# Kernel optimization log

Hardware: AMD Instinct MI355X
Metric: run time of the kernel (lower is better)

The kernel has to match this reference:

```python
import jax, jax.numpy as jnp
import numpy as np

SX, SY, C, K = 256, 256, 3, 15
DD, DT, SIGMA = 5, 0.2, 0.65
C0 = tuple(i % C for i in range(K))
C1 = tuple(tuple(i for i in range(K) if i % C == c) for c in range(C))
MA = DD - SIGMA  # flow magnitude bound


def _sobel(A):
    # A: (X, Y, c) -> (X, Y, 2, c); matches jsp.signal.convolve2d(..., mode='same')
    kx = jnp.array([[1., 0., -1.], [2., 0., -2.], [1., 0., -1.]], dtype=A.dtype)
    ky = kx.T
    # convolve2d flips the kernel; emulate true convolution by correlating with rot180 kernels
    kern = jnp.stack([jnp.rot90(ky, 2), jnp.rot90(kx, 2)])[:, None]  # (2,1,3,3): [grad_y, grad_x]
    x = jnp.transpose(A, (2, 0, 1))[:, None]                          # (c,1,X,Y)
    out = jax.lax.conv_general_dilated(x, kern, (1, 1), 'SAME')       # (c,2,X,Y)
    return jnp.transpose(out, (2, 3, 1, 0))                           # (X,Y,2,c)


def _reintegration(A, P, F):
    # Reintegration tracking, has_hidden=True, border='wall', mix='softmax'
    xs, ys = jnp.meshgrid(jnp.arange(SX), jnp.arange(SY))
    pos = (jnp.dstack((ys, xs)) + .5).astype(A.dtype)     # (X,Y,2) cell centers (row, col)
    mus = pos[..., None] + jnp.clip(DT * F, -MA, MA)      # (X,Y,2,C) target centers
    mus = jnp.clip(mus, SIGMA, SX - SIGMA)                # wall border
    shifts = jnp.array([(dx, dy) for dx in range(-DD, DD + 1) for dy in range(-DD, DD + 1)])
    cap = min(1., 2 * SIGMA)

    def step(sft):
        sh = (sft[0], sft[1])
        Ar = jnp.roll(A, sh, axis=(0, 1))
        Pr = jnp.roll(P, sh, axis=(0, 1))
        mur = jnp.roll(mus, sh, axis=(0, 1))
        dpmu = jnp.abs(pos[..., None] - mur)              # (X,Y,2,C)
        sz = .5 - dpmu + SIGMA
        area = jnp.prod(jnp.clip(sz, 0., cap), axis=2) / (4 * SIGMA ** 2)  # (X,Y,C)
        return Ar * area, Pr

    nA, nP = jax.vmap(step)(shifts)                       # (N,X,Y,C), (N,X,Y,K)
    expnA = jnp.exp(nA.sum(-1, keepdims=True)) - 1.       # softmax mix rule
    newA = nA.sum(0)
    newP = (nP * expnA).sum(0) / (expnA.sum(0) + 1e-10)
    return newA, newP


def _forward(A, P, fK_real, fK_imag, m, s):
    fK = fK_real + 1j * fK_imag                           # (X,Y,K) kernel FFTs
    fA = jnp.fft.fft2(A, axes=(0, 1))                     # (X,Y,C)
    fAk = jnp.take(fA, jnp.array(C0), axis=2)             # (X,Y,K) per-kernel source channel
    U = jnp.real(jnp.fft.ifft2(fK * fAk, axes=(0, 1)))    # (X,Y,K)
    U = (2. * jnp.exp(-((U - m) ** 2) / (2. * s ** 2)) - 1.) * P  # growth(U,m,s)*P
    U = jnp.dstack([U[:, :, C1[c]].sum(-1) for c in range(C)])    # (X,Y,C)
    F = _sobel(U)                                         # (X,Y,2,C)
    Cg = _sobel(A.sum(-1, keepdims=True))                 # (X,Y,2,1)
    alpha = jnp.clip((A[:, :, None, :] / 2.) ** 2, 0., 1.)
    F = jnp.clip(F * (1. - alpha) - Cg * alpha, -MA, MA)
    return _reintegration(A, P, F)


def setup_inputs() -> dict:
    key = jax.random.key(0)
    kA, kP, kr, km, ks, ka, kb, kw = jax.random.split(key, 8)
    A = jax.random.uniform(kA, (SX, SY, C), dtype=jnp.float32)
    P = jax.random.uniform(kP, (SX, SY, K), dtype=jnp.float32)
    R = 15.0
    r = jax.random.uniform(kr, (K,), minval=.2, maxval=1.)
    m = jax.random.uniform(km, (K,), minval=.05, maxval=.5, dtype=jnp.float32)
    s = jax.random.uniform(ks, (K,), minval=.001, maxval=.18, dtype=jnp.float32)
    a = jax.random.uniform(ka, (K, 3))
    b = jax.random.uniform(kb, (K, 3), minval=.001, maxval=1.)
    w = jax.random.uniform(kw, (K, 3), minval=.01, maxval=.5)
    mid = SX // 2
    D = jnp.linalg.norm(jnp.mgrid[-mid:mid, -mid:mid], axis=0)[..., None] / ((R + 15.) * r)  # (X,Y,K)
    Kk = jax.nn.sigmoid(-(D - 1.) * 10.) * (b * jnp.exp(-((D[..., None] - a) / w) ** 2)).sum(-1)
    nK = Kk / Kk.sum((0, 1), keepdims=True)
    fK = jnp.fft.fft2(jnp.fft.fftshift(nK, axes=(0, 1)), axes=(0, 1))
    return {"A": A, "P": P,
            "fK_real": jnp.real(fK).astype(jnp.float32),
            "fK_imag": jnp.imag(fK).astype(jnp.float32),
            "m": m, "s": s}


def reference(A, P, fK_real, fK_imag, m, s):
    return _forward(A, P, fK_real, fK_imag, m, s)
```

## Files before the change

kernel.cpp:

```cpp
#include <hip/hip_runtime.h>


#define SXY 256
#define XY  65536
#define NC  3
#define NK  15

__device__ __forceinline__ float2 cmul(float2 a, float2 b) {
  return make_float2(a.x * b.x - a.y * b.y, a.x * b.y + a.y * b.x);
}

__device__ __forceinline__ void fft256_lds(float2* b0, float2* b1, int t, float sign) {
  float2* src = b0;
  float2* dst = b1;
#pragma unroll
  for (int stage = 0; stage < 4; ++stage) {
    __syncthreads();
    const int Ns = 1 << (2 * stage);
    float2 v0 = src[t];
    float2 v1 = src[t + 64];
    float2 v2 = src[t + 128];
    float2 v3 = src[t + 192];
    const int jm = t & (Ns - 1);
    float ang = sign * 6.283185307179586f * (float)jm / (float)(Ns * 4);
    float sn, cs;
    __sincosf(ang, &sn, &cs);
    float2 w1 = make_float2(cs, sn);
    float2 w2 = cmul(w1, w1);
    float2 w3 = cmul(w2, w1);
    v1 = cmul(v1, w1);
    v2 = cmul(v2, w2);
    v3 = cmul(v3, w3);
    float2 a0 = make_float2(v0.x + v2.x, v0.y + v2.y);
    float2 a1 = make_float2(v0.x - v2.x, v0.y - v2.y);
    float2 a2 = make_float2(v1.x + v3.x, v1.y + v3.y);
    float2 a3 = make_float2(v1.x - v3.x, v1.y - v3.y);
    float2 ia3 = make_float2(-sign * a3.y, sign * a3.x);
    const int idxD = ((t >> (2 * stage)) << (2 * stage)) * 4 + jm;
    dst[idxD]          = make_float2(a0.x + a2.x, a0.y + a2.y);
    dst[idxD + Ns]     = make_float2(a1.x + ia3.x, a1.y + ia3.y);
    dst[idxD + 2 * Ns] = make_float2(a0.x - a2.x, a0.y - a2.y);
    dst[idxD + 3 * Ns] = make_float2(a1.x - ia3.x, a1.y - ia3.y);
    float2* tmp = src; src = dst; dst = tmp;
  }
  __syncthreads();
}

__global__ __launch_bounds__(64) void k_rowfft(const float* __restrict__ A,
                                               float2* __restrict__ RF) {
  __shared__ float2 b0[256], b1[256];
  const int t = threadIdx.x;
  const int x = blockIdx.x & 255;
  const int c = blockIdx.x >> 8;
#pragma unroll
  for (int r = 0; r < 4; ++r) {
    int y = t + 64 * r;
    b0[y] = make_float2(A[(x * 256 + y) * NC + c], 0.0f);
  }
  fft256_lds(b0, b1, t, -1.0f);
#pragma unroll
  for (int r = 0; r < 4; ++r) {
    int y = t + 64 * r;
    RF[(c * 256 + x) * 256 + y] = b0[y];
  }
}

__global__ __launch_bounds__(64) void k_colfft(const float* __restrict__ fKr,
                                               const float* __restrict__ fKi,
                                               const float2* __restrict__ RF,
                                               float2* __restrict__ T2) {
  __shared__ float2 b0[256], b1[256];
  const int t = threadIdx.x;
  const int y = blockIdx.x & 255;
  const int c = blockIdx.x >> 8;
#pragma unroll
  for (int r = 0; r < 4; ++r) {
    int x = t + 64 * r;
    b0[x] = RF[(c * 256 + x) * 256 + y];
  }
  fft256_lds(b0, b1, t, -1.0f);
  float2 fa[4];
#pragma unroll
  for (int r = 0; r < 4; ++r) fa[r] = b0[t + 64 * r];
  for (int j = 0; j < 5; ++j) {
    const int k = c + 3 * j;
#pragma unroll
    for (int r = 0; r < 4; ++r) {
      int x = t + 64 * r;
      float2 Kv = make_float2(fKr[(x * 256 + y) * NK + k], fKi[(x * 256 + y) * NK + k]);
      b0[x] = cmul(Kv, fa[r]);
    }
    fft256_lds(b0, b1, t, 1.0f);
#pragma unroll
    for (int r = 0; r < 4; ++r) {
      int x = t + 64 * r;
      T2[(k * 256 + x) * 256 + y] = b0[x];
    }
  }
}

__global__ __launch_bounds__(64) void k_irowfft_growth(const float2* __restrict__ T2,
                                                       const float* __restrict__ P,
                                                       const float* __restrict__ m,
                                                       const float* __restrict__ s,
                                                       float* __restrict__ Ucol) {
  __shared__ float2 b0[256], b1[256];
  const int t = threadIdx.x;
  const int x = blockIdx.x & 255;
  const int c = blockIdx.x >> 8;
  float acc[4] = {0.f, 0.f, 0.f, 0.f};
  for (int j = 0; j < 5; ++j) {
    const int k = c + 3 * j;
    const float mk = m[k];
    const float sk = s[k];
    const float inv2s2 = 0.5f / (sk * sk);
#pragma unroll
    for (int r = 0; r < 4; ++r) {
      int y = t + 64 * r;
      b0[y] = T2[(k * 256 + x) * 256 + y];
    }
    fft256_lds(b0, b1, t, 1.0f);
#pragma unroll
    for (int q = 0; q < 4; ++q) {
      int y = t + 64 * q;
      float U = b0[y].x * (1.0f / 65536.0f);
      float d = U - mk;
      float g = 2.0f * __expf(-d * d * inv2s2) - 1.0f;
      acc[q] += g * P[(x * 256 + y) * NK + k];
    }
  }
#pragma unroll
  for (int q = 0; q < 4; ++q) {
    int y = t + 64 * q;
    Ucol[(c * 256 + x) * 256 + y] = acc[q];
  }
}

__global__ __launch_bounds__(256) void k_flow(const float* __restrict__ A,
                                              const float* __restrict__ Ucol,
                                              float* __restrict__ F) {
  const int idx = blockIdx.x * 256 + threadIdx.x;
  const int x = idx >> 8;
  const int y = idx & 255;
  const float MA = 4.35f;

  float u[3][3][3];
  float asum[3][3];
#pragma unroll
  for (int di = -1; di <= 1; ++di) {
#pragma unroll
    for (int dj = -1; dj <= 1; ++dj) {
      int xi = x + di, yj = y + dj;
      bool inb = ((unsigned)xi < 256u) && ((unsigned)yj < 256u);
      float a0 = 0.f, a1 = 0.f, a2 = 0.f, as = 0.f;
      if (inb) {
        int b = xi * 256 + yj;
        a0 = Ucol[0 * XY + b];
        a1 = Ucol[1 * XY + b];
        a2 = Ucol[2 * XY + b];
        const float* ap = A + b * NC;
        as = ap[0] + ap[1] + ap[2];
      }
      u[0][di + 1][dj + 1] = a0;
      u[1][di + 1][dj + 1] = a1;
      u[2][di + 1][dj + 1] = a2;
      asum[di + 1][dj + 1] = as;
    }
  }
  float cg0 = (asum[2][0] + 2.f * asum[2][1] + asum[2][2]) -
              (asum[0][0] + 2.f * asum[0][1] + asum[0][2]);
  float cg1 = (asum[0][2] + 2.f * asum[1][2] + asum[2][2]) -
              (asum[0][0] + 2.f * asum[1][0] + asum[2][0]);
  const int b = x * 256 + y;
#pragma unroll
  for (int c = 0; c < NC; ++c) {
    float f0 = (u[c][2][0] + 2.f * u[c][2][1] + u[c][2][2]) -
               (u[c][0][0] + 2.f * u[c][0][1] + u[c][0][2]);
    float f1 = (u[c][0][2] + 2.f * u[c][1][2] + u[c][2][2]) -
               (u[c][0][0] + 2.f * u[c][1][0] + u[c][2][0]);
    float ah = A[b * NC + c] * 0.5f;
    float al = fminf(ah * ah, 1.0f);
    f0 = fminf(fmaxf(f0 * (1.f - al) - cg0 * al, -MA), MA);
    f1 = fminf(fmaxf(f1 * (1.f - al) - cg1 * al, -MA), MA);
    F[(b * 2 + 0) * NC + c] = f0;
    F[(b * 2 + 1) * NC + c] = f1;
  }
}

__global__ __launch_bounds__(256) void k_reint(const float* __restrict__ A,
                                               const float* __restrict__ P,
                                               const float* __restrict__ F,
                                               float* __restrict__ outA,
                                               float* __restrict__ outP) {
  const int idx = blockIdx.x * 256 + threadIdx.x;
  const int x = idx >> 8;
  const int y = idx & 255;
  const float SIGMA = 0.65f;
  const float INV4S2 = 1.0f / (4.0f * 0.65f * 0.65f);
  const float DT = 0.2f;
  const float px = x + 0.5f;
  const float py = y + 0.5f;

  float accA[3] = {0.f, 0.f, 0.f};
  float accP[15];
#pragma unroll
  for (int k = 0; k < NK; ++k) accP[k] = 0.f;
  float esum = 0.f;

  for (int dx = -2; dx <= 2; ++dx) {
    for (int dy = -2; dy <= 2; ++dy) {
      const int sx = (x - dx) & 255;
      const int sy = (y - dy) & 255;
      const int sb = sx * 256 + sy;
      const float spx = sx + 0.5f;
      const float spy = sy + 0.5f;
      float sumnA = 0.f;
      float nAc[3];
#pragma unroll
      for (int c = 0; c < NC; ++c) {
        float f0 = F[(sb * 2 + 0) * NC + c];
        float f1 = F[(sb * 2 + 1) * NC + c];
        float mu0 = fminf(fmaxf(spx + DT * f0, SIGMA), 256.f - SIGMA);
        float mu1 = fminf(fmaxf(spy + DT * f1, SIGMA), 256.f - SIGMA);
        float sz0 = 0.5f - fabsf(px - mu0) + SIGMA;
        float sz1 = 0.5f - fabsf(py - mu1) + SIGMA;
        sz0 = fminf(fmaxf(sz0, 0.f), 1.f);
        sz1 = fminf(fmaxf(sz1, 0.f), 1.f);
        float area = sz0 * sz1 * INV4S2;
        float na = A[sb * NC + c] * area;
        nAc[c] = na;
        sumnA += na;
      }
      float e = __expf(sumnA) - 1.0f;
      accA[0] += nAc[0];
      accA[1] += nAc[1];
      accA[2] += nAc[2];
      esum += e;
      const float* pp = P + sb * NK;
#pragma unroll
      for (int k = 0; k < NK; ++k) accP[k] += pp[k] * e;
    }
  }
  const int b = x * 256 + y;
#pragma unroll
  for (int c = 0; c < NC; ++c) outA[b * NC + c] = accA[c];
  const float inv = 1.0f / (esum + 1e-10f);
#pragma unroll
  for (int k = 0; k < NK; ++k) outP[b * NK + k] = accP[k] * inv;
}

extern "C" void kernel_launch(void* const* d_in, const int* in_sizes, int n_in,
                              void* d_out, int out_size, void* d_ws, size_t ws_size,
                              hipStream_t stream) {
  const float* A   = (const float*)d_in[0];
  const float* P   = (const float*)d_in[1];
  const float* fKr = (const float*)d_in[2];
  const float* fKi = (const float*)d_in[3];
  const float* m   = (const float*)d_in[4];
  const float* s   = (const float*)d_in[5];

  float* ws = (float*)d_ws;
  float2* RF   = (float2*)ws;
  float2* T2   = RF + NC * XY;
  float*  Ucol = (float*)(T2 + NK * XY);
  float*  F    = Ucol + NC * XY;

  float* outA = (float*)d_out;
  float* outP = outA + NC * XY;

  k_rowfft<<<NC * 256, 64, 0, stream>>>(A, RF);
  k_colfft<<<NC * 256, 64, 0, stream>>>(fKr, fKi, RF, T2);
  k_irowfft_growth<<<NC * 256, 64, 0, stream>>>(T2, P, m, s, Ucol);
  k_flow<<<256, 256, 0, stream>>>(A, Ucol, F);
  k_reint<<<256, 256, 0, stream>>>(A, P, F, outA, outP);
}
```

Measured before the change: 120.4 us.

## Batch column FFTs per 8 columns and parallelize kernel channels across waves

```diff
diff --git a/kernel.cpp b/kernel.cpp
--- a/kernel.cpp
+++ b/kernel.cpp
@@ -1,10 +1,10 @@
 #include <hip/hip_runtime.h>
 
 
-#define SXY 256
 #define XY  65536
 #define NC  3
 #define NK  15
+#define WPAD 260
 
 __device__ __forceinline__ float2 cmul(float2 a, float2 b) {
   return make_float2(a.x * b.x - a.y * b.y, a.x * b.y + a.y * b.x);
@@ -65,74 +65,101 @@
   }
 }
 
-__global__ __launch_bounds__(64) void k_colfft(const float* __restrict__ fKr,
-                                               const float* __restrict__ fKi,
-                                               const float2* __restrict__ RF,
-                                               float2* __restrict__ T2) {
-  __shared__ float2 b0[256], b1[256];
-  const int t = threadIdx.x;
-  const int y = blockIdx.x & 255;
-  const int c = blockIdx.x >> 8;
-#pragma unroll
-  for (int r = 0; r < 4; ++r) {
-    int x = t + 64 * r;
-    b0[x] = RF[(c * 256 + x) * 256 + y];
-  }
-  fft256_lds(b0, b1, t, -1.0f);
+__global__ __launch_bounds__(512, 1) void k_colfft(const float* __restrict__ fKr,
+                                                   const float* __restrict__ fKi,
+                                                   const float2* __restrict__ RF,
+                                                   float2* __restrict__ T2) {
+  __shared__ float2 lds0[8 * WPAD];
+  __shared__ float2 lds1[8 * WPAD];
+  const int tid = threadIdx.x;
+  const int k = blockIdx.x >> 5;
+  const int y0 = (blockIdx.x & 31) << 3;
+  const int c = k % 3;
+
+  {
+    const int q = tid & 3;
+#pragma unroll
+    for (int r = 0; r < 2; ++r) {
+      const int x = (tid >> 2) + (r << 7);
+      const float4* src = (const float4*)(RF + (c * XY + x * 256 + y0));
+      float4 v = src[q];
+      lds0[(2 * q) * WPAD + x]     = make_float2(v.x, v.y);
+      lds0[(2 * q + 1) * WPAD + x] = make_float2(v.z, v.w);
+    }
+  }
+
+  const int w = tid >> 6, lane = tid & 63;
+  float2* b0 = lds0 + w * WPAD;
+  float2* b1 = lds1 + w * WPAD;
+  fft256_lds(b0, b1, lane, -1.0f);
+
+  const int y = y0 + w;
   float2 fa[4];
 #pragma unroll
-  for (int r = 0; r < 4; ++r) fa[r] = b0[t + 64 * r];
-  for (int j = 0; j < 5; ++j) {
-    const int k = c + 3 * j;
-#pragma unroll
-    for (int r = 0; r < 4; ++r) {
-      int x = t + 64 * r;
-      float2 Kv = make_float2(fKr[(x * 256 + y) * NK + k], fKi[(x * 256 + y) * NK + k]);
-      b0[x] = cmul(Kv, fa[r]);
+  for (int r = 0; r < 4; ++r) fa[r] = b0[lane + 64 * r];
+#pragma unroll
+  for (int r = 0; r < 4; ++r) {
+    const int x = lane + 64 * r;
+    const int fi = (x * 256 + y) * NK + k;
+    float2 Kv = make_float2(fKr[fi], fKi[fi]);
+    b0[x] = cmul(Kv, fa[r]);
+  }
+  fft256_lds(b0, b1, lane, 1.0f);
+
+  {
+    const int q = tid & 3;
+#pragma unroll
+    for (int r = 0; r < 2; ++r) {
+      const int x = (tid >> 2) + (r << 7);
+      float2 v0 = lds0[(2 * q) * WPAD + x];
+      float2 v1 = lds0[(2 * q + 1) * WPAD + x];
+      float4* dst = (float4*)(T2 + (k * XY + x * 256 + y0));
+      dst[q] = make_float4(v0.x, v0.y, v1.x, v1.y);
     }
-    fft256_lds(b0, b1, t, 1.0f);
-#pragma unroll
-    for (int r = 0; r < 4; ++r) {
-      int x = t + 64 * r;
-      T2[(k * 256 + x) * 256 + y] = b0[x];
-    }
-  }
-}
-
-__global__ __launch_bounds__(64) void k_irowfft_growth(const float2* __restrict__ T2,
-                                                       const float* __restrict__ P,
-                                                       const float* __restrict__ m,
-                                                       const float* __restrict__ s,
-                                                       float* __restrict__ Ucol) {
-  __shared__ float2 b0[256], b1[256];
-  const int t = threadIdx.x;
+  }
+}
+
+__global__ __launch_bounds__(320, 1) void k_irowfft_growth(const float2* __restrict__ T2,
+                                                           const float* __restrict__ P,
+                                                           const float* __restrict__ m,
+                                                           const float* __restrict__ s,
+                                                           float* __restrict__ Ucol) {
+  __shared__ float2 lds0[5 * WPAD];
+  __shared__ float2 lds1[5 * WPAD];
+  __shared__ float accs[5 * WPAD];
+  const int tid = threadIdx.x;
   const int x = blockIdx.x & 255;
   const int c = blockIdx.x >> 8;
-  float acc[4] = {0.f, 0.f, 0.f, 0.f};
-  for (int j = 0; j < 5; ++j) {
-    const int k = c + 3 * j;
-    const float mk = m[k];
-    const float sk = s[k];
-    const float inv2s2 = 0.5f / (sk * sk);
-#pragma unroll
-    for (int r = 0; r < 4; ++r) {
-      int y = t + 64 * r;
-      b0[y] = T2[(k * 256 + x) * 256 + y];
-    }
-    fft256_lds(b0, b1, t, 1.0f);
-#pragma unroll
-    for (int q = 0; q < 4; ++q) {
-      int y = t + 64 * q;
-      float U = b0[y].x * (1.0f / 65536.0f);
-      float d = U - mk;
-      float g = 2.0f * __expf(-d * d * inv2s2) - 1.0f;
-      acc[q] += g * P[(x * 256 + y) * NK + k];
-    }
-  }
-#pragma unroll
-  for (int q = 0; q < 4; ++q) {
-    int y = t + 64 * q;
-    Ucol[(c * 256 + x) * 256 + y] = acc[q];
+  const int j = tid >> 6, lane = tid & 63;
+  const int k = c + 3 * j;
+
+  float2* b0 = lds0 + j * WPAD;
+  float2* b1 = lds1 + j * WPAD;
+  const float2* src = T2 + (k * XY + x * 256);
+#pragma unroll
+  for (int r = 0; r < 4; ++r) {
+    int y = lane + 64 * r;
+    b0[y] = src[y];
+  }
+  fft256_lds(b0, b1, lane, 1.0f);
+
+  const float mk = m[k];
+  const float sk = s[k];
+  const float inv2s2 = 0.5f / (sk * sk);
+#pragma unroll
+  for (int r = 0; r < 4; ++r) {
+    int y = lane + 64 * r;
+    float U = b0[y].x * (1.0f / 65536.0f);
+    float d = U - mk;
+    float g = 2.0f * __expf(-d * d * inv2s2) - 1.0f;
+    accs[j * WPAD + y] = g * P[(x * 256 + y) * NK + k];
+  }
+  __syncthreads();
+  if (tid < 256) {
+    float sum = 0.f;
+#pragma unroll
+    for (int j2 = 0; j2 < 5; ++j2) sum += accs[j2 * WPAD + tid];
+    Ucol[c * XY + x * 256 + tid] = sum;
   }
 }
 
@@ -269,8 +296,8 @@
   float* outP = outA + NC * XY;
 
   k_rowfft<<<NC * 256, 64, 0, stream>>>(A, RF);
-  k_colfft<<<NC * 256, 64, 0, stream>>>(fKr, fKi, RF, T2);
-  k_irowfft_growth<<<NC * 256, 64, 0, stream>>>(T2, P, m, s, Ucol);
+  k_colfft<<<NK * 32, 512, 0, stream>>>(fKr, fKi, RF, T2);
+  k_irowfft_growth<<<NC * 256, 320, 0, stream>>>(T2, P, m, s, Ucol);
   k_flow<<<256, 256, 0, stream>>>(A, Ucol, F);
   k_reint<<<256, 256, 0, stream>>>(A, P, F, outA, outP);
 }
```

Result: faster. 107.3 us (-10.8%).
